# Kernel tuning notes

Measured on AMD Instinct MI355X. Metric: run time of the kernel, lower is better.

## Reference

```python
import jax, jax.numpy as jnp
import numpy as np

B, T, IN, HID, NC = 1024, 128, 512, 1024, 10

def setup_inputs() -> dict:
    key = jax.random.key(0)
    ks = jax.random.split(key, 4)
    x = jax.random.normal(ks[0], (B, T, IN), dtype=jnp.float32)
    Wxh = jax.random.normal(ks[1], (IN, HID), dtype=jnp.float32) * (1.0 / np.sqrt(IN))
    b_xh = jnp.zeros((HID,), dtype=jnp.float32)
    Whh = jax.random.normal(ks[2], (HID, HID), dtype=jnp.float32) * (1.0 / np.sqrt(HID))
    b_hh = jnp.zeros((HID,), dtype=jnp.float32)
    Why = jax.random.normal(ks[3], (HID, NC), dtype=jnp.float32) * (1.0 / np.sqrt(HID))
    b_y = jnp.zeros((NC,), dtype=jnp.float32)
    return {"x": x, "Wxh": Wxh, "b_xh": b_xh, "Whh": Whh, "b_hh": b_hh, "Why": Why, "b_y": b_y}

def reference(x, Wxh, b_xh, Whh, b_hh, Why, b_y):
    # Precompute input projections for all timesteps in one big GEMM: [B,T,HID]
    xproj = jnp.einsum('bti,ih->bth', x, Wxh) + b_xh
    h0 = jnp.zeros((x.shape[0], Whh.shape[0]), dtype=x.dtype)
    def step(h, xp_t):
        h = jnp.tanh(xp_t + h @ Whh + b_hh)
        return h, None
    hT, _ = jax.lax.scan(step, h0, jnp.swapaxes(xproj, 0, 1))  # scan over T
    return hT @ Why + b_y
```

## Files before the change

kernel.cpp:

```cpp
#include <hip/hip_runtime.h>
#include <hip/hip_bf16.h>

#define TT    128
#define BATCH 1024
#define INDIM 512
#define HIDD  1024
#define NCLS  10

typedef __bf16 bf16x8 __attribute__((ext_vector_type(8)));
typedef float  f32x4  __attribute__((ext_vector_type(4)));
typedef unsigned short u16x8 __attribute__((ext_vector_type(8)));

__device__ __forceinline__ unsigned short bf16b(float f) {
    __hip_bfloat16 h = __float2bfloat16(f);
    return __builtin_bit_cast(unsigned short, h);
}

__device__ __forceinline__ float tanh_fast(float x) {
    float e = __expf(2.0f * x);
    return 1.0f - 2.0f * __builtin_amdgcn_rcpf(e + 1.0f);
}

#define WAITV(n) asm volatile("s_waitcnt vmcnt(" #n ")" ::: "memory")
#define WAITL()  asm volatile("s_waitcnt lgkmcnt(0)" ::: "memory")
#define BAR()    asm volatile("s_barrier" ::: "memory")

__global__ __launch_bounds__(256) void prep_kernel(
    const float* __restrict__ Whh, const float* __restrict__ Wxh,
    __hip_bfloat16* __restrict__ WhhT_hi, __hip_bfloat16* __restrict__ WhhT_lo,
    __hip_bfloat16* __restrict__ WxhT_hi, __hip_bfloat16* __restrict__ WxhT_lo)
{
    __shared__ float tl[64][68];
    int bid = blockIdx.x, tid = threadIdx.x;
    const float* src; int N, k0, n0, dstride;
    __hip_bfloat16 *dhi, *dlo;
    if (bid < 256) { src = Whh; N = 1024; k0 = (bid >> 4) << 6; n0 = (bid & 15) << 6;
                     dhi = WhhT_hi; dlo = WhhT_lo; dstride = 1024; }
    else { int b = bid - 256; src = Wxh; N = 1024; k0 = (b >> 4) << 6; n0 = (b & 15) << 6;
           dhi = WxhT_hi; dlo = WxhT_lo; dstride = 512; }

    int r = tid >> 2, c0 = (tid & 3) << 4;
    const float* s = src + (size_t)(k0 + r) * N + n0 + c0;
#pragma unroll
    for (int j = 0; j < 4; ++j)
        *(float4*)&tl[r][c0 + j * 4] = *(const float4*)(s + j * 4);
    __syncthreads();

    int rn = tid >> 2, ck0 = (tid & 3) << 4;
    u16x8 hi0, hi1, lo0, lo1;
#pragma unroll
    for (int j = 0; j < 16; ++j) {
        float w = tl[ck0 + j][rn];
        unsigned short hb = bf16b(w);
        float hf = __bfloat162float(__builtin_bit_cast(__hip_bfloat16, hb));
        unsigned short lb = bf16b(w - hf);
        if (j < 8) { hi0[j] = hb; lo0[j] = lb; }
        else       { hi1[j - 8] = hb; lo1[j - 8] = lb; }
    }
    size_t o = (size_t)(n0 + rn) * dstride + k0 + ck0;
    *(u16x8*)(void*)(dhi + o)     = hi0;
    *(u16x8*)(void*)(dhi + o + 8) = hi1;
    *(u16x8*)(void*)(dlo + o)     = lo0;
    *(u16x8*)(void*)(dlo + o + 8) = lo1;
}

__global__ __launch_bounds__(256) void convx_all_kernel(
    const float* __restrict__ x, __hip_bfloat16* __restrict__ xs)
{
    size_t gid = (size_t)blockIdx.x * 256 + threadIdx.x;
    int i  = (int)(gid & 63) << 3;
    size_t bt = gid >> 6;
    int t = (int)(bt & 127);
    int b = (int)(bt >> 7);
    const float* s = x + ((size_t)b * TT + t) * INDIM + i;
    float4 a0 = *(const float4*)s, a1 = *(const float4*)(s + 4);
    u16x8 o;
    o[0]=bf16b(a0.x); o[1]=bf16b(a0.y); o[2]=bf16b(a0.z); o[3]=bf16b(a0.w);
    o[4]=bf16b(a1.x); o[5]=bf16b(a1.y); o[6]=bf16b(a1.z); o[7]=bf16b(a1.w);
    *(u16x8*)(void*)(xs + ((size_t)t * BATCH + b) * INDIM + i) = o;
}

__global__ __launch_bounds__(256) void zero_kernel(
    __hip_bfloat16* __restrict__ h, unsigned* __restrict__ bar)
{
    if (blockIdx.x < 512) {
        size_t i = ((size_t)blockIdx.x * 256 + threadIdx.x) << 3;
        u16x8 z = {0,0,0,0,0,0,0,0};
        *(u16x8*)(void*)(h + i) = z;
    } else {
        uint4 z = {0,0,0,0};
#pragma unroll
        for (int k = 0; k < 8; ++k)
            ((uint4*)bar)[k * 256 + threadIdx.x] = z;
    }
}

#define BUF(i) (smem + ((i) << 14))

#define FRAGA(_b, m, ks) \
    (*(const bf16x8*)((_b) + ((((m)<<4)+ar) << 8) + ((((((ks)<<2)+kg)) ^ (ar & 7)) << 4)))

#define STAGE(basePtr, rs, bufidx, AUX) do {                                   \
    _Pragma("unroll")                                                          \
    for (int _i = 0; _i < 4; ++_i) {                                           \
        int _r = (_i << 4) + (tid >> 4);                                       \
        int _s = (tid & 15) ^ (_r & 7);                                        \
        const void* _g = (const void*)((basePtr) + (size_t)_r * (rs) + (_s << 3)); \
        void* _l = (void*)(smem + ((bufidx) << 14) + (_i << 12) + (wave << 10));   \
        __builtin_amdgcn_global_load_lds(                                      \
            (const __attribute__((address_space(1))) void*)_g,                 \
            (__attribute__((address_space(3))) void*)_l, 16, 0, AUX);          \
    } } while (0)

#define MF(a_, b_, c_) c_ = __builtin_amdgcn_mfma_f32_16x16x32_bf16(a_, b_, c_, 0,0,0)

#define DO_CHUNK_H(q, bufptr) do {                                             \
    const char* _b = (const char*)(bufptr);                                    \
    _Pragma("unroll")                                                          \
    for (int _ks = 0; _ks < 4; ++_ks) {                                        \
        bf16x8 a0 = FRAGA(_b, 0, _ks), a1 = FRAGA(_b, 1, _ks);                 \
        bf16x8 a2 = FRAGA(_b, 2, _ks), a3 = FRAGA(_b, 3, _ks);                 \
        bf16x8 b00 = Bh[(q)*16 + _ks*4 + 0], b01 = Bh[(q)*16 + _ks*4 + 2];     \
        bf16x8 b10 = Bh[(q)*16 + _ks*4 + 1], b11 = Bh[(q)*16 + _ks*4 + 3];     \
        MF(a0, b00, acc00); MF(a1, b00, acc10);                                \
        MF(a2, b00, acc20); MF(a3, b00, acc30);                                \
        MF(a0, b01, acc01); MF(a1, b01, acc11);                                \
        MF(a2, b01, acc21); MF(a3, b01, acc31);                                \
        MF(a0, b10, acc00); MF(a1, b10, acc10);                                \
        MF(a2, b10, acc20); MF(a3, b10, acc30);                                \
        MF(a0, b11, acc01); MF(a1, b11, acc11);                                \
        MF(a2, b11, acc21); MF(a3, b11, acc31);                                \
    } } while (0)

#define DO_CHUNK_X(q, bufptr) do {                                             \
    const char* _b = (const char*)(bufptr);                                    \
    _Pragma("unroll")                                                          \
    for (int _ks = 0; _ks < 4; ++_ks) {                                        \
        bf16x8 a0 = FRAGA(_b, 0, _ks), a1 = FRAGA(_b, 1, _ks);                 \
        bf16x8 a2 = FRAGA(_b, 2, _ks), a3 = FRAGA(_b, 3, _ks);                 \
        bf16x8 bx0 = Bx[(q)*8 + _ks*2 + 0], bx1 = Bx[(q)*8 + _ks*2 + 1];       \
        MF(a0, bx0, acc00); MF(a1, bx0, acc10);                                \
        MF(a2, bx0, acc20); MF(a3, bx0, acc30);                                \
        MF(a0, bx1, acc01); MF(a1, bx1, acc11);                                \
        MF(a2, bx1, acc21); MF(a3, bx1, acc31);                                \
    } } while (0)

__global__ __launch_bounds__(256, 1) void rnn_kernel(
    __hip_bfloat16* __restrict__ h0, __hip_bfloat16* __restrict__ h1,
    const __hip_bfloat16* __restrict__ xs,
    const __hip_bfloat16* __restrict__ WhhT_hi, const __hip_bfloat16* __restrict__ WhhT_lo,
    const __hip_bfloat16* __restrict__ WxhT_hi, const __hip_bfloat16* __restrict__ WxhT_lo,
    const float* __restrict__ b_xh, const float* __restrict__ b_hh,
    unsigned* __restrict__ bar)
{
    __shared__ char smem[147456];
    int tid = threadIdx.x, bid = blockIdx.x;
    int by = (bid & 7) | (((bid >> 3) & 1) << 3);
    int bx = bid >> 4;
    int lane = tid & 63, wave = tid >> 6;
    int kh = wave & 1, nh = wave >> 1;
    int ar = lane & 15, kg = lane >> 4;
    int bx64 = bx << 6, by64 = by << 6;

    bf16x8 Bh[64], Bx[16];
    float bias0, bias1;
    {
        int col0 = bx64 + (nh << 5) + ar;
        bias0 = b_xh[col0] + b_hh[col0];
        bias1 = b_xh[col0 + 16] + b_hh[col0 + 16];
#pragma unroll
        for (int cg = 0; cg < 2; ++cg) {
            int col = bx64 + (nh << 5) + (cg << 4) + ar;
#pragma unroll
            for (int q = 0; q < 4; ++q)
#pragma unroll
                for (int ks = 0; ks < 4; ++ks) {
                    int k = (((kh << 2) + q) << 7) + (ks << 5) + (kg << 3);
                    Bh[q*16 + ks*4 + cg*2 + 0] = *(const bf16x8*)(WhhT_hi + (size_t)col * HIDD + k);
                    Bh[q*16 + ks*4 + cg*2 + 1] = *(const bf16x8*)(WhhT_lo + (size_t)col * HIDD + k);
                }
#pragma unroll
            for (int q = 0; q < 2; ++q)
#pragma unroll
                for (int ks = 0; ks < 4; ++ks) {
                    int k = (((kh << 1) + q) << 7) + (ks << 5) + (kg << 3);
                    Bx[q*8 + ks*2 + cg] = *(const bf16x8*)(WxhT_hi + (size_t)col * INDIM + k);
                }
        }
    }

    unsigned* grpflags = bar + (by << 9);
    unsigned* myflag   = grpflags + (bx << 5);

    {
        const __hip_bfloat16* xA0 = xs + (size_t)by64 * INDIM;
        STAGE(xA0 + 0*128, INDIM, 0, 0);
        STAGE(xA0 + 1*128, INDIM, 1, 0);
        STAGE(xA0 + 2*128, INDIM, 2, 0);
        STAGE(xA0 + 3*128, INDIM, 3, 0);
    }
    WAITV(0); BAR();

    for (int t = 0; t < TT; ++t) {
        const __hip_bfloat16* hA = (t & 1) ? h1 : h0;
        __hip_bfloat16*       hB = (t & 1) ? h0 : h1;
        const __hip_bfloat16* hR = hA + (size_t)by64 * HIDD;
        const __hip_bfloat16* xN = xs + (size_t)(t + 1) * (BATCH * INDIM)
                                      + (size_t)by64 * INDIM;
        int nl = (t < TT - 1);

        f32x4 acc00 = {0,0,0,0}, acc01 = {0,0,0,0};
        f32x4 acc10 = {0,0,0,0}, acc11 = {0,0,0,0};
        f32x4 acc20 = {0,0,0,0}, acc21 = {0,0,0,0};
        f32x4 acc30 = {0,0,0,0}, acc31 = {0,0,0,0};

        if (kh == 0) { DO_CHUNK_X(0, BUF(0)); DO_CHUNK_X(1, BUF(1)); }
        else         { DO_CHUNK_X(0, BUF(2)); DO_CHUNK_X(1, BUF(3)); }

        if (t > 0 && wave == 0) {
            unsigned tgt = (unsigned)t;
            for (;;) {
                unsigned v = tgt;
                if (lane < 16)
                    v = __hip_atomic_load(grpflags + (lane << 5), __ATOMIC_RELAXED,
                                          __HIP_MEMORY_SCOPE_AGENT);
                if (__all(v >= tgt)) break;
                __builtin_amdgcn_s_sleep(1);
            }
        }
        BAR();

        STAGE(hR + 0*128, HIDD, 4, 1);
        STAGE(hR + 1*128, HIDD, 5, 1);
        STAGE(hR + 4*128, HIDD, 6, 1);
        STAGE(hR + 5*128, HIDD, 7, 1);
        if (nl) {
            STAGE(xN + 0*128, INDIM, 0, 0);
            STAGE(xN + 1*128, INDIM, 1, 0);
            STAGE(xN + 2*128, INDIM, 2, 0);
            STAGE(xN + 3*128, INDIM, 3, 0);
            WAITV(16);
        } else {
            WAITV(0);
        }
        BAR();

        if (kh == 0) { DO_CHUNK_H(0, BUF(4)); DO_CHUNK_H(1, BUF(5)); }
        else         { DO_CHUNK_H(0, BUF(6)); DO_CHUNK_H(1, BUF(7)); }
        BAR();

        STAGE(hR + 2*128, HIDD, 4, 1);
        STAGE(hR + 3*128, HIDD, 5, 1);
        STAGE(hR + 6*128, HIDD, 6, 1);
        STAGE(hR + 7*128, HIDD, 7, 1);
        WAITV(0);
        BAR();

        if (kh == 0) { DO_CHUNK_H(2, BUF(4)); DO_CHUNK_H(3, BUF(5)); }
        else         { DO_CHUNK_H(2, BUF(6)); DO_CHUNK_H(3, BUF(7)); }

        {
            char* pw = smem + (8 << 14) + (wave << 12);
            if (kh == 0) {
                *(f32x4*)(pw +    0 + (lane << 4)) = acc20;
                *(f32x4*)(pw + 1024 + (lane << 4)) = acc21;
                *(f32x4*)(pw + 2048 + (lane << 4)) = acc30;
                *(f32x4*)(pw + 3072 + (lane << 4)) = acc31;
            } else {
                *(f32x4*)(pw +    0 + (lane << 4)) = acc00;
                *(f32x4*)(pw + 1024 + (lane << 4)) = acc01;
                *(f32x4*)(pw + 2048 + (lane << 4)) = acc10;
                *(f32x4*)(pw + 3072 + (lane << 4)) = acc11;
            }
        }
        WAITL(); BAR();

        {
            const char* pr = smem + (8 << 14) + ((wave ^ 1) << 12);
            f32x4 p0 = *(const f32x4*)(pr +    0 + (lane << 4));
            f32x4 p1 = *(const f32x4*)(pr + 1024 + (lane << 4));
            f32x4 p2 = *(const f32x4*)(pr + 2048 + (lane << 4));
            f32x4 p3 = *(const f32x4*)(pr + 3072 + (lane << 4));
            int colb = bx64 + (nh << 5) + ar;
            if (kh == 0) {
                acc00 += p0; acc01 += p1; acc10 += p2; acc11 += p3;
#pragma unroll
                for (int j = 0; j < 4; ++j) {
                    int r0 = by64 + (kg << 2) + j;
                    hB[(size_t)r0 * HIDD + colb]             = __float2bfloat16(tanh_fast(acc00[j] + bias0));
                    hB[(size_t)r0 * HIDD + colb + 16]        = __float2bfloat16(tanh_fast(acc01[j] + bias1));
                    hB[(size_t)(r0 + 16) * HIDD + colb]      = __float2bfloat16(tanh_fast(acc10[j] + bias0));
                    hB[(size_t)(r0 + 16) * HIDD + colb + 16] = __float2bfloat16(tanh_fast(acc11[j] + bias1));
                }
            } else {
                acc20 += p0; acc21 += p1; acc30 += p2; acc31 += p3;
#pragma unroll
                for (int j = 0; j < 4; ++j) {
                    int r0 = by64 + 32 + (kg << 2) + j;
                    hB[(size_t)r0 * HIDD + colb]             = __float2bfloat16(tanh_fast(acc20[j] + bias0));
                    hB[(size_t)r0 * HIDD + colb + 16]        = __float2bfloat16(tanh_fast(acc21[j] + bias1));
                    hB[(size_t)(r0 + 16) * HIDD + colb]      = __float2bfloat16(tanh_fast(acc30[j] + bias0));
                    hB[(size_t)(r0 + 16) * HIDD + colb + 16] = __float2bfloat16(tanh_fast(acc31[j] + bias1));
                }
            }
        }
        WAITV(0);
        BAR();
        if (nl && tid == 0)
            __hip_atomic_store(myflag, (unsigned)(t + 1), __ATOMIC_RELAXED,
                               __HIP_MEMORY_SCOPE_AGENT);
    }
}

__global__ __launch_bounds__(64) void out_kernel(
    const __hip_bfloat16* __restrict__ h, const float* __restrict__ Why,
    const float* __restrict__ b_y, float* __restrict__ out)
{
    int b = blockIdx.x, lane = threadIdx.x;
    float acc[NCLS];
#pragma unroll
    for (int c = 0; c < NCLS; ++c) acc[c] = 0.f;
    for (int kk = 0; kk < 16; ++kk) {
        int k = (kk << 6) + lane;
        float hv = __bfloat162float(h[(size_t)b * HIDD + k]);
#pragma unroll
        for (int c = 0; c < NCLS; ++c) acc[c] += hv * Why[(size_t)k * NCLS + c];
    }
#pragma unroll
    for (int c = 0; c < NCLS; ++c) {
        float v = acc[c];
#pragma unroll
        for (int off = 32; off > 0; off >>= 1) v += __shfl_down(v, off);
        if (lane == 0) out[(size_t)b * NCLS + c] = v + b_y[c];
    }
}

extern "C" void kernel_launch(void* const* d_in, const int* in_sizes, int n_in,
                              void* d_out, int out_size, void* d_ws, size_t ws_size,
                              hipStream_t stream)
{
    const float* x    = (const float*)d_in[0];
    const float* Wxh  = (const float*)d_in[1];
    const float* b_xh = (const float*)d_in[2];
    const float* Whh  = (const float*)d_in[3];
    const float* b_hh = (const float*)d_in[4];
    const float* Why  = (const float*)d_in[5];
    const float* b_y  = (const float*)d_in[6];
    float* out = (float*)d_out;

    char* ws = (char*)d_ws;
    __hip_bfloat16* WhhT_hi = (__hip_bfloat16*)(ws);
    __hip_bfloat16* WhhT_lo = (__hip_bfloat16*)(ws + (2u  << 20));
    __hip_bfloat16* WxhT_hi = (__hip_bfloat16*)(ws + (4u  << 20));
    __hip_bfloat16* WxhT_lo = (__hip_bfloat16*)(ws + (5u  << 20));
    __hip_bfloat16* h0      = (__hip_bfloat16*)(ws + (6u  << 20));
    __hip_bfloat16* h1      = (__hip_bfloat16*)(ws + (8u  << 20));
    unsigned*       bar     = (unsigned*)      (ws + (10u << 20));
    __hip_bfloat16* xs      = (__hip_bfloat16*)(ws + (16u << 20));

    prep_kernel<<<384, 256, 0, stream>>>(Whh, Wxh, WhhT_hi, WhhT_lo, WxhT_hi, WxhT_lo);
    convx_all_kernel<<<32768, 256, 0, stream>>>(x, xs);
    zero_kernel<<<513, 256, 0, stream>>>(h0, bar);

    rnn_kernel<<<256, 256, 0, stream>>>(h0, h1, xs,
                                        WhhT_hi, WhhT_lo, WxhT_hi, WxhT_lo,
                                        b_xh, b_hh, bar);

    out_kernel<<<1024, 64, 0, stream>>>(h0, Why, b_y, out);
}
```

Measured before the change: 880.6 us.

## Split persistent RNN block into eight waves with four-way K split and LDS reduction

Doubles threads per block from 256 to 512, so each wave handles a quarter of the K dimension. This halves the per-wave register-resident Whh/Wxh fragments and MFMA work per step. The two-way partial-sum exchange becomes a four-way LDS reduction in which each K-group finalizes 16 rows. The aim is more latency hiding and shorter per-step critical paths in the latency-bound recurrence, at the cost of more LDS reduction traffic and barrier participants. The launch_bounds of (512,2) may also constrain register allocation.

```diff
diff --git a/kernel.cpp b/kernel.cpp
--- a/kernel.cpp
+++ b/kernel.cpp
@@ -102,11 +102,11 @@
 
 #define STAGE(basePtr, rs, bufidx, AUX) do {                                   \
     _Pragma("unroll")                                                          \
-    for (int _i = 0; _i < 4; ++_i) {                                           \
-        int _r = (_i << 4) + (tid >> 4);                                       \
+    for (int _i = 0; _i < 2; ++_i) {                                           \
+        int _r = (_i << 5) + (tid >> 4);                                       \
         int _s = (tid & 15) ^ (_r & 7);                                        \
         const void* _g = (const void*)((basePtr) + (size_t)_r * (rs) + (_s << 3)); \
-        void* _l = (void*)(smem + ((bufidx) << 14) + (_i << 12) + (wave << 10));   \
+        void* _l = (void*)(smem + ((bufidx) << 14) + (_i << 13) + (wave << 10));   \
         __builtin_amdgcn_global_load_lds(                                      \
             (const __attribute__((address_space(1))) void*)_g,                 \
             (__attribute__((address_space(3))) void*)_l, 16, 0, AUX);          \
@@ -120,32 +120,35 @@
     for (int _ks = 0; _ks < 4; ++_ks) {                                        \
         bf16x8 a0 = FRAGA(_b, 0, _ks), a1 = FRAGA(_b, 1, _ks);                 \
         bf16x8 a2 = FRAGA(_b, 2, _ks), a3 = FRAGA(_b, 3, _ks);                 \
-        bf16x8 b00 = Bh[(q)*16 + _ks*4 + 0], b01 = Bh[(q)*16 + _ks*4 + 2];     \
-        bf16x8 b10 = Bh[(q)*16 + _ks*4 + 1], b11 = Bh[(q)*16 + _ks*4 + 3];     \
-        MF(a0, b00, acc00); MF(a1, b00, acc10);                                \
-        MF(a2, b00, acc20); MF(a3, b00, acc30);                                \
-        MF(a0, b01, acc01); MF(a1, b01, acc11);                                \
-        MF(a2, b01, acc21); MF(a3, b01, acc31);                                \
-        MF(a0, b10, acc00); MF(a1, b10, acc10);                                \
-        MF(a2, b10, acc20); MF(a3, b10, acc30);                                \
-        MF(a0, b11, acc01); MF(a1, b11, acc11);                                \
-        MF(a2, b11, acc21); MF(a3, b11, acc31);                                \
+        bf16x8 h00 = Bh[(q)*16 + _ks*4 + 0], h01 = Bh[(q)*16 + _ks*4 + 2];     \
+        bf16x8 h10 = Bh[(q)*16 + _ks*4 + 1], h11 = Bh[(q)*16 + _ks*4 + 3];     \
+        MF(a0, h00, acc00); MF(a1, h00, acc10);                                \
+        MF(a2, h00, acc20); MF(a3, h00, acc30);                                \
+        MF(a0, h01, acc01); MF(a1, h01, acc11);                                \
+        MF(a2, h01, acc21); MF(a3, h01, acc31);                                \
+        MF(a0, h10, acc00); MF(a1, h10, acc10);                                \
+        MF(a2, h10, acc20); MF(a3, h10, acc30);                                \
+        MF(a0, h11, acc01); MF(a1, h11, acc11);                                \
+        MF(a2, h11, acc21); MF(a3, h11, acc31);                                \
     } } while (0)
 
-#define DO_CHUNK_X(q, bufptr) do {                                             \
+#define DO_CHUNK_X(bufptr) do {                                                \
     const char* _b = (const char*)(bufptr);                                    \
     _Pragma("unroll")                                                          \
     for (int _ks = 0; _ks < 4; ++_ks) {                                        \
         bf16x8 a0 = FRAGA(_b, 0, _ks), a1 = FRAGA(_b, 1, _ks);                 \
         bf16x8 a2 = FRAGA(_b, 2, _ks), a3 = FRAGA(_b, 3, _ks);                 \
-        bf16x8 bx0 = Bx[(q)*8 + _ks*2 + 0], bx1 = Bx[(q)*8 + _ks*2 + 1];       \
-        MF(a0, bx0, acc00); MF(a1, bx0, acc10);                                \
-        MF(a2, bx0, acc20); MF(a3, bx0, acc30);                                \
-        MF(a0, bx1, acc01); MF(a1, bx1, acc11);                                \
-        MF(a2, bx1, acc21); MF(a3, bx1, acc31);                                \
+        bf16x8 x0 = Bx[_ks*2 + 0], x1 = Bx[_ks*2 + 1];                         \
+        MF(a0, x0, acc00); MF(a1, x0, acc10);                                  \
+        MF(a2, x0, acc20); MF(a3, x0, acc30);                                  \
+        MF(a0, x1, acc01); MF(a1, x1, acc11);                                  \
+        MF(a2, x1, acc21); MF(a3, x1, acc31);                                  \
     } } while (0)
 
-__global__ __launch_bounds__(256, 1) void rnn_kernel(
+#define REDT(cg_, m_, j_) \
+    (smem + (4 << 14) + (((((nh << 1) | (cg_)) << 4) | (((m_) << 2) | (j_))) << 10) + (lane << 4))
+
+__global__ __launch_bounds__(512, 2) void rnn_kernel(
     __hip_bfloat16* __restrict__ h0, __hip_bfloat16* __restrict__ h1,
     const __hip_bfloat16* __restrict__ xs,
     const __hip_bfloat16* __restrict__ WhhT_hi, const __hip_bfloat16* __restrict__ WhhT_lo,
@@ -158,11 +161,11 @@
     int by = (bid & 7) | (((bid >> 3) & 1) << 3);
     int bx = bid >> 4;
     int lane = tid & 63, wave = tid >> 6;
-    int kh = wave & 1, nh = wave >> 1;
+    int kh = wave >> 1, nh = wave & 1;
     int ar = lane & 15, kg = lane >> 4;
     int bx64 = bx << 6, by64 = by << 6;
 
-    bf16x8 Bh[64], Bx[16];
+    bf16x8 Bh[32], Bx[8];
     float bias0, bias1;
     {
         int col0 = bx64 + (nh << 5) + ar;
@@ -172,20 +175,18 @@
         for (int cg = 0; cg < 2; ++cg) {
             int col = bx64 + (nh << 5) + (cg << 4) + ar;
 #pragma unroll
-            for (int q = 0; q < 4; ++q)
+            for (int q = 0; q < 2; ++q)
 #pragma unroll
                 for (int ks = 0; ks < 4; ++ks) {
-                    int k = (((kh << 2) + q) << 7) + (ks << 5) + (kg << 3);
+                    int k = (((kh << 1) + q) << 7) + (ks << 5) + (kg << 3);
                     Bh[q*16 + ks*4 + cg*2 + 0] = *(const bf16x8*)(WhhT_hi + (size_t)col * HIDD + k);
                     Bh[q*16 + ks*4 + cg*2 + 1] = *(const bf16x8*)(WhhT_lo + (size_t)col * HIDD + k);
                 }
 #pragma unroll
-            for (int q = 0; q < 2; ++q)
-#pragma unroll
-                for (int ks = 0; ks < 4; ++ks) {
-                    int k = (((kh << 1) + q) << 7) + (ks << 5) + (kg << 3);
-                    Bx[q*8 + ks*2 + cg] = *(const bf16x8*)(WxhT_hi + (size_t)col * INDIM + k);
-                }
+            for (int ks = 0; ks < 4; ++ks) {
+                int k = (kh << 7) + (ks << 5) + (kg << 3);
+                Bx[ks*2 + cg] = *(const bf16x8*)(WxhT_hi + (size_t)col * INDIM + k);
+            }
         }
     }
 
@@ -214,8 +215,7 @@
         f32x4 acc20 = {0,0,0,0}, acc21 = {0,0,0,0};
         f32x4 acc30 = {0,0,0,0}, acc31 = {0,0,0,0};
 
-        if (kh == 0) { DO_CHUNK_X(0, BUF(0)); DO_CHUNK_X(1, BUF(1)); }
-        else         { DO_CHUNK_X(0, BUF(2)); DO_CHUNK_X(1, BUF(3)); }
+        DO_CHUNK_X(BUF(kh));
 
         if (t > 0 && wave == 0) {
             unsigned tgt = (unsigned)t;
@@ -231,77 +231,73 @@
         BAR();
 
         STAGE(hR + 0*128, HIDD, 4, 1);
-        STAGE(hR + 1*128, HIDD, 5, 1);
+        STAGE(hR + 2*128, HIDD, 5, 1);
         STAGE(hR + 4*128, HIDD, 6, 1);
-        STAGE(hR + 5*128, HIDD, 7, 1);
+        STAGE(hR + 6*128, HIDD, 7, 1);
         if (nl) {
             STAGE(xN + 0*128, INDIM, 0, 0);
             STAGE(xN + 1*128, INDIM, 1, 0);
             STAGE(xN + 2*128, INDIM, 2, 0);
             STAGE(xN + 3*128, INDIM, 3, 0);
-            WAITV(16);
+            WAITV(8);
         } else {
             WAITV(0);
         }
         BAR();
 
-        if (kh == 0) { DO_CHUNK_H(0, BUF(4)); DO_CHUNK_H(1, BUF(5)); }
-        else         { DO_CHUNK_H(0, BUF(6)); DO_CHUNK_H(1, BUF(7)); }
-        BAR();
-
-        STAGE(hR + 2*128, HIDD, 4, 1);
+        DO_CHUNK_H(0, BUF(4 + kh));
+        BAR();
+
+        STAGE(hR + 1*128, HIDD, 4, 1);
         STAGE(hR + 3*128, HIDD, 5, 1);
-        STAGE(hR + 6*128, HIDD, 6, 1);
+        STAGE(hR + 5*128, HIDD, 6, 1);
         STAGE(hR + 7*128, HIDD, 7, 1);
         WAITV(0);
         BAR();
 
-        if (kh == 0) { DO_CHUNK_H(2, BUF(4)); DO_CHUNK_H(3, BUF(5)); }
-        else         { DO_CHUNK_H(2, BUF(6)); DO_CHUNK_H(3, BUF(7)); }
+        DO_CHUNK_H(1, BUF(4 + kh));
+        BAR();
+
+        if (kh == 0) {
+            *(f32x4*)REDT(0,1,0) = acc10; *(f32x4*)REDT(1,1,0) = acc11;
+            *(f32x4*)REDT(0,2,0) = acc20; *(f32x4*)REDT(1,2,0) = acc21;
+            *(f32x4*)REDT(0,3,0) = acc30; *(f32x4*)REDT(1,3,0) = acc31;
+        } else if (kh == 1) {
+            *(f32x4*)REDT(0,0,1) = acc00; *(f32x4*)REDT(1,0,1) = acc01;
+            *(f32x4*)REDT(0,2,1) = acc20; *(f32x4*)REDT(1,2,1) = acc21;
+            *(f32x4*)REDT(0,3,1) = acc30; *(f32x4*)REDT(1,3,1) = acc31;
+        } else if (kh == 2) {
+            *(f32x4*)REDT(0,0,2) = acc00; *(f32x4*)REDT(1,0,2) = acc01;
+            *(f32x4*)REDT(0,1,2) = acc10; *(f32x4*)REDT(1,1,2) = acc11;
+            *(f32x4*)REDT(0,3,2) = acc30; *(f32x4*)REDT(1,3,2) = acc31;
+        } else {
+            *(f32x4*)REDT(0,0,3) = acc00; *(f32x4*)REDT(1,0,3) = acc01;
+            *(f32x4*)REDT(0,1,3) = acc10; *(f32x4*)REDT(1,1,3) = acc11;
+            *(f32x4*)REDT(0,2,3) = acc20; *(f32x4*)REDT(1,2,3) = acc21;
+        }
+        WAITL(); BAR();
 
         {
-            char* pw = smem + (8 << 14) + (wave << 12);
+            f32x4 s0, s1;
             if (kh == 0) {
-                *(f32x4*)(pw +    0 + (lane << 4)) = acc20;
-                *(f32x4*)(pw + 1024 + (lane << 4)) = acc21;
-                *(f32x4*)(pw + 2048 + (lane << 4)) = acc30;
-                *(f32x4*)(pw + 3072 + (lane << 4)) = acc31;
+                s0 = acc00 + *(const f32x4*)REDT(0,0,1) + *(const f32x4*)REDT(0,0,2) + *(const f32x4*)REDT(0,0,3);
+                s1 = acc01 + *(const f32x4*)REDT(1,0,1) + *(const f32x4*)REDT(1,0,2) + *(const f32x4*)REDT(1,0,3);
+            } else if (kh == 1) {
+                s0 = acc10 + *(const f32x4*)REDT(0,1,0) + *(const f32x4*)REDT(0,1,2) + *(const f32x4*)REDT(0,1,3);
+                s1 = acc11 + *(const f32x4*)REDT(1,1,0) + *(const f32x4*)REDT(1,1,2) + *(const f32x4*)REDT(1,1,3);
+            } else if (kh == 2) {
+                s0 = acc20 + *(const f32x4*)REDT(0,2,0) + *(const f32x4*)REDT(0,2,1) + *(const f32x4*)REDT(0,2,3);
+                s1 = acc21 + *(const f32x4*)REDT(1,2,0) + *(const f32x4*)REDT(1,2,1) + *(const f32x4*)REDT(1,2,3);
             } else {
-                *(f32x4*)(pw +    0 + (lane << 4)) = acc00;
-                *(f32x4*)(pw + 1024 + (lane << 4)) = acc01;
-                *(f32x4*)(pw + 2048 + (lane << 4)) = acc10;
-                *(f32x4*)(pw + 3072 + (lane << 4)) = acc11;
+                s0 = acc30 + *(const f32x4*)REDT(0,3,0) + *(const f32x4*)REDT(0,3,1) + *(const f32x4*)REDT(0,3,2);
+                s1 = acc31 + *(const f32x4*)REDT(1,3,0) + *(const f32x4*)REDT(1,3,1) + *(const f32x4*)REDT(1,3,2);
             }
-        }
-        WAITL(); BAR();
-
-        {
-            const char* pr = smem + (8 << 14) + ((wave ^ 1) << 12);
-            f32x4 p0 = *(const f32x4*)(pr +    0 + (lane << 4));
-            f32x4 p1 = *(const f32x4*)(pr + 1024 + (lane << 4));
-            f32x4 p2 = *(const f32x4*)(pr + 2048 + (lane << 4));
-            f32x4 p3 = *(const f32x4*)(pr + 3072 + (lane << 4));
             int colb = bx64 + (nh << 5) + ar;
-            if (kh == 0) {
-                acc00 += p0; acc01 += p1; acc10 += p2; acc11 += p3;
-#pragma unroll
-                for (int j = 0; j < 4; ++j) {
-                    int r0 = by64 + (kg << 2) + j;
-                    hB[(size_t)r0 * HIDD + colb]             = __float2bfloat16(tanh_fast(acc00[j] + bias0));
-                    hB[(size_t)r0 * HIDD + colb + 16]        = __float2bfloat16(tanh_fast(acc01[j] + bias1));
-                    hB[(size_t)(r0 + 16) * HIDD + colb]      = __float2bfloat16(tanh_fast(acc10[j] + bias0));
-                    hB[(size_t)(r0 + 16) * HIDD + colb + 16] = __float2bfloat16(tanh_fast(acc11[j] + bias1));
-                }
-            } else {
-                acc20 += p0; acc21 += p1; acc30 += p2; acc31 += p3;
-#pragma unroll
-                for (int j = 0; j < 4; ++j) {
-                    int r0 = by64 + 32 + (kg << 2) + j;
-                    hB[(size_t)r0 * HIDD + colb]             = __float2bfloat16(tanh_fast(acc20[j] + bias0));
-                    hB[(size_t)r0 * HIDD + colb + 16]        = __float2bfloat16(tanh_fast(acc21[j] + bias1));
-                    hB[(size_t)(r0 + 16) * HIDD + colb]      = __float2bfloat16(tanh_fast(acc30[j] + bias0));
-                    hB[(size_t)(r0 + 16) * HIDD + colb + 16] = __float2bfloat16(tanh_fast(acc31[j] + bias1));
-                }
+#pragma unroll
+            for (int j = 0; j < 4; ++j) {
+                int row = by64 + (kh << 4) + (kg << 2) + j;
+                hB[(size_t)row * HIDD + colb]      = __float2bfloat16(tanh_fast(s0[j] + bias0));
+                hB[(size_t)row * HIDD + colb + 16] = __float2bfloat16(tanh_fast(s1[j] + bias1));
             }
         }
         WAITV(0);
@@ -362,7 +358,7 @@
     convx_all_kernel<<<32768, 256, 0, stream>>>(x, xs);
     zero_kernel<<<513, 256, 0, stream>>>(h0, bar);
 
-    rnn_kernel<<<256, 256, 0, stream>>>(h0, h1, xs,
+    rnn_kernel<<<256, 512, 0, stream>>>(h0, h1, xs,
                                         WhhT_hi, WhhT_lo, WxhT_hi, WxhT_lo,
                                         b_xh, b_hh, bar);
 
```

Measured after the change: 854.4 us. -3.0%, faster.
